# Performance work log

Measured on AMD Instinct MI355X. Metric: run time of the kernel, lower is better.

Reference implementation:

```python
import jax, jax.numpy as jnp
import numpy as np

B, T, C, H = 4, 2048, 1024, 16


def setup_inputs() -> dict:
    key = jax.random.key(0)
    k0, k1, k2 = jax.random.split(key, 3)
    s = C ** -0.5
    return {
        "x": jax.random.normal(k0, (B, T, C), jnp.float32),
        "Wqkv": jax.random.normal(k1, (C, 3 * C), jnp.float32) * s,
        "bqkv": jnp.zeros((3 * C,), jnp.float32),
        "Wo": jax.random.normal(k2, (C, C), jnp.float32) * s,
        "bo": jnp.zeros((C,), jnp.float32),
        "decoder": 1,
    }


def reference(x, Wqkv, bqkv, Wo, bo, decoder):
    Bx, Tx, Cx = x.shape
    d = Cx // H  # head dim
    qkv = x @ Wqkv + bqkv  # [B,T,3C]
    q, k, v = jnp.split(qkv, 3, axis=-1)
    q = q.reshape(Bx, Tx, H, d).transpose(0, 2, 1, 3)  # [B,H,T,d]
    k = k.reshape(Bx, Tx, H, d).transpose(0, 2, 1, 3)
    v = v.reshape(Bx, Tx, H, d).transpose(0, 2, 1, 3)
    # Source: qk / embd_dim**(-0.5)  ==  qk * sqrt(embd_dim)  (faithful quirk)
    scale = jnp.asarray(Cx ** 0.5, x.dtype)
    qk = jnp.einsum("bhqd,bhkd->bhqk", q, k) * scale  # [B,H,T,T]
    if decoder:  # decoder is a Python int constant
        tril = jnp.tril(jnp.ones((Tx, Tx), bool))
        qk = jnp.where(tril, qk, -jnp.inf)
    attn = jax.nn.softmax(qk, axis=-1)
    out = jnp.einsum("bhqk,bhkd->bhqd", attn, v)  # [B,H,T,d]
    out = out.transpose(0, 2, 1, 3).reshape(Bx, Tx, Cx)
    return out @ Wo + bo
```

## Files before the change

### kernel.cpp

```cpp
#include <hip/hip_runtime.h>
#include <cstdint>
#include <cstddef>

#define T_SEQ 2048
#define CEMB  1024
#define NHEAD 16
#define DHEAD 64

typedef __attribute__((ext_vector_type(8))) short bf16x8;
typedef __attribute__((ext_vector_type(4))) float f32x4;

static __device__ __forceinline__ unsigned short f2bf(float x) {
    unsigned u = __builtin_bit_cast(unsigned, x);
    unsigned r = (u + 0x7FFFu + ((u >> 16) & 1u)) >> 16;
    return (unsigned short)r;
}
static __device__ __forceinline__ float bf2f(unsigned short b) {
    unsigned u = ((unsigned)b) << 16;
    return __builtin_bit_cast(float, u);
}

static __device__ __forceinline__ void gload16(const short* gsrc, short* ldsbase) {
    __builtin_amdgcn_global_load_lds(
        (const __attribute__((address_space(1))) void*)gsrc,
        (__attribute__((address_space(3))) void*)ldsbase, 16, 0, 0);
}

template<int SPLIT, bool A_F32, bool OUT_BF16>
__global__ __launch_bounds__(256) void gemm_mfma_kernel(
    const float* __restrict__ Af,
    const short* __restrict__ Ah,
    const short* __restrict__ Bh,
    const short* __restrict__ Bl,
    const float* __restrict__ bias,
    void* __restrict__ Cout, int K, int ldc)
{
    __shared__ __align__(16) short smem[(SPLIT == 3) ? 16384 : 8192];

    const int tid = threadIdx.x;
    const int w = tid >> 6, l = tid & 63;
    const int lr = l & 15, lg = l >> 4;
    const int wr = w >> 1, wc = w & 1;
    const int row0 = blockIdx.y * 128;
    const int col0 = blockIdx.x * 128;

    f32x4 acc[4][4];
    #pragma unroll
    for (int mt = 0; mt < 4; ++mt)
        #pragma unroll
        for (int nt = 0; nt < 4; ++nt)
            acc[mt][nt] = (f32x4){0.f, 0.f, 0.f, 0.f};

    const int sB0 = w * 128 + l, sB1 = sB0 + 64;
    const short* gB0 = Bh + (size_t)(col0 + (sB0 & 127)) * K + (sB0 >> 7) * 8;
    const short* gB1 = Bh + (size_t)(col0 + (sB1 & 127)) * K + (sB1 >> 7) * 8;
    short* dB0 = &smem[4096 + (w * 128) * 8];
    short* dB1 = &smem[4096 + (w * 128 + 64) * 8];
    const short* gBl0 = nullptr; const short* gBl1 = nullptr;
    if constexpr (SPLIT == 3) {
        gBl0 = Bl + (size_t)(col0 + (sB0 & 127)) * K + (sB0 >> 7) * 8;
        gBl1 = Bl + (size_t)(col0 + (sB1 & 127)) * K + (sB1 >> 7) * 8;
    }

    const short* gA0 = nullptr; const short* gA1 = nullptr;
    if constexpr (!A_F32) {
        gA0 = Ah + (size_t)(row0 + (sB0 & 127)) * K + (sB0 >> 7) * 8;
        gA1 = Ah + (size_t)(row0 + (sB1 & 127)) * K + (sB1 >> 7) * 8;
    }
    short* dA0 = &smem[(w * 128) * 8];
    short* dA1 = &smem[(w * 128 + 64) * 8];

    const int arow = tid >> 1, ahalf = tid & 1;
    const float* gAf = A_F32 ? (Af + (size_t)(row0 + arow) * K + ahalf * 16) : nullptr;

    for (int kt = 0; kt < K; kt += 32) {
        __syncthreads();
        if constexpr (!A_F32) {
            gload16(gA0 + kt, dA0);
            gload16(gA1 + kt, dA1);
        }
        gload16(gB0 + kt, dB0);
        gload16(gB1 + kt, dB1);
        if constexpr (SPLIT == 3) {
            gload16(gBl0 + kt, &smem[12288 + (w * 128) * 8]);
            gload16(gBl1 + kt, &smem[12288 + (w * 128 + 64) * 8]);
        }
        if constexpr (A_F32) {
            const float* src = gAf + kt;
            float4 f0 = *(const float4*)(src);
            float4 f1 = *(const float4*)(src + 4);
            float4 f2 = *(const float4*)(src + 8);
            float4 f3 = *(const float4*)(src + 12);
            float xs[16] = {f0.x, f0.y, f0.z, f0.w, f1.x, f1.y, f1.z, f1.w,
                            f2.x, f2.y, f2.z, f2.w, f3.x, f3.y, f3.z, f3.w};
            #pragma unroll
            for (int q = 0; q < 2; ++q) {
                bf16x8 h8, l8;
                #pragma unroll
                for (int e = 0; e < 8; ++e) {
                    float x = xs[q * 8 + e];
                    if constexpr (SPLIT == 3) {
                        unsigned u = __builtin_bit_cast(unsigned, x);
                        h8[e] = (short)(unsigned short)(u >> 16);
                        float hf = __builtin_bit_cast(float, u & 0xFFFF0000u);
                        l8[e] = (short)f2bf(x - hf);
                    } else {
                        h8[e] = (short)f2bf(x);
                    }
                }
                int slot = (ahalf * 2 + q) * 128 + arow;
                *(bf16x8*)&smem[slot * 8] = h8;
                if constexpr (SPLIT == 3) *(bf16x8*)&smem[8192 + slot * 8] = l8;
            }
        }
        __syncthreads();

        const int aoff = (lg * 128 + wr * 64 + lr) * 8;
        const int boff = 4096 + (lg * 128 + wc * 64 + lr) * 8;
        bf16x8 ahf[4], alf[4];
        #pragma unroll
        for (int mt = 0; mt < 4; ++mt) {
            ahf[mt] = *(const bf16x8*)&smem[aoff + mt * 128];
            if constexpr (SPLIT == 3)
                alf[mt] = *(const bf16x8*)&smem[8192 + aoff + mt * 128];
        }
        #pragma unroll
        for (int nt = 0; nt < 4; ++nt) {
            bf16x8 bhf = *(const bf16x8*)&smem[boff + nt * 128];
            if constexpr (SPLIT == 3) {
                bf16x8 blf = *(const bf16x8*)&smem[8192 + boff + nt * 128];
                #pragma unroll
                for (int mt = 0; mt < 4; ++mt) {
                    acc[mt][nt] = __builtin_amdgcn_mfma_f32_16x16x32_bf16(ahf[mt], bhf, acc[mt][nt], 0, 0, 0);
                    acc[mt][nt] = __builtin_amdgcn_mfma_f32_16x16x32_bf16(alf[mt], bhf, acc[mt][nt], 0, 0, 0);
                    acc[mt][nt] = __builtin_amdgcn_mfma_f32_16x16x32_bf16(ahf[mt], blf, acc[mt][nt], 0, 0, 0);
                }
            } else {
                #pragma unroll
                for (int mt = 0; mt < 4; ++mt)
                    acc[mt][nt] = __builtin_amdgcn_mfma_f32_16x16x32_bf16(ahf[mt], bhf, acc[mt][nt], 0, 0, 0);
            }
        }
    }

    #pragma unroll
    for (int mt = 0; mt < 4; ++mt) {
        #pragma unroll
        for (int r = 0; r < 4; ++r) {
            int m = row0 + wr * 64 + mt * 16 + lg * 4 + r;
            #pragma unroll
            for (int nt = 0; nt < 4; ++nt) {
                int n = col0 + wc * 64 + nt * 16 + lr;
                float v = acc[mt][nt][r] + bias[n];
                if constexpr (OUT_BF16)
                    ((short*)Cout)[(size_t)m * ldc + n] = (short)f2bf(v);
                else
                    ((float*)Cout)[(size_t)m * ldc + n] = v;
            }
        }
    }
}

__global__ __launch_bounds__(256) void transpose_split_kernel(
    const float* __restrict__ src, int nsrc,
    short* __restrict__ hi, short* __restrict__ lo)
{
    __shared__ float tile[64][68];
    const int tid = threadIdx.x;
    const int n0 = blockIdx.x * 64, k0 = blockIdx.y * 64;
    {
        int kr = tid >> 2, cg = tid & 3;
        const float* s = src + (size_t)(k0 + kr) * nsrc + n0 + cg * 16;
        #pragma unroll
        for (int q = 0; q < 4; ++q) {
            float4 f = *(const float4*)(s + q * 4);
            tile[kr][cg * 16 + q * 4 + 0] = f.x;
            tile[kr][cg * 16 + q * 4 + 1] = f.y;
            tile[kr][cg * 16 + q * 4 + 2] = f.z;
            tile[kr][cg * 16 + q * 4 + 3] = f.w;
        }
    }
    __syncthreads();
    {
        int nr = tid >> 2, kg = tid & 3;
        int n = n0 + nr;
        bf16x8 h0, h1, lo0, lo1;
        #pragma unroll
        for (int e = 0; e < 8; ++e) {
            float a = tile[kg * 16 + e][nr];
            float b = tile[kg * 16 + 8 + e][nr];
            unsigned short ha = f2bf(a), hb = f2bf(b);
            h0[e] = (short)ha; h1[e] = (short)hb;
            lo0[e] = (short)f2bf(a - bf2f(ha));
            lo1[e] = (short)f2bf(b - bf2f(hb));
        }
        short* dh = hi + (size_t)n * 1024 + k0 + kg * 16;
        *(bf16x8*)dh = h0;
        *(bf16x8*)(dh + 8) = h1;
        if (lo) {
            short* dl = lo + (size_t)n * 1024 + k0 + kg * 16;
            *(bf16x8*)dl = lo0;
            *(bf16x8*)(dl + 8) = lo1;
        }
    }
}

__global__ __launch_bounds__(256) void repack_vt_kernel(
    const short* __restrict__ v, short* __restrict__ vt)
{
    __shared__ short tile[64][80];
    const int tid = threadIdx.x;
    const int tt = blockIdx.x, h = blockIdx.y, b = blockIdx.z;
    const int t0 = tt * 64;
    {
        int tr = tid >> 2, cgrp = tid & 3;
        const short* src = v + (size_t)(b * T_SEQ + t0 + tr) * CEMB + h * DHEAD + cgrp * 16;
        *(bf16x8*)&tile[tr][cgrp * 16]     = *(const bf16x8*)src;
        *(bf16x8*)&tile[tr][cgrp * 16 + 8] = *(const bf16x8*)(src + 8);
    }
    __syncthreads();
    {
        int d = tid >> 2, tc = tid & 3;
        short s[16];
        #pragma unroll
        for (int e = 0; e < 16; ++e) s[e] = tile[tc * 16 + e][d];
        short* dst = vt + ((size_t)((b * NHEAD + h) * DHEAD + d)) * T_SEQ + t0 + tc * 16;
        bf16x8 v0, v1;
        #pragma unroll
        for (int e = 0; e < 8; ++e) { v0[e] = s[e]; v1[e] = s[8 + e]; }
        *(bf16x8*)dst       = v0;
        *(bf16x8*)(dst + 8) = v1;
    }
}

__global__ __launch_bounds__(256) void attn_mfma_kernel(
    const float* __restrict__ qk, const short* __restrict__ vt,
    short* __restrict__ ctxb)
{
    __shared__ __align__(16) short K_hi[64 * 64];
    __shared__ __align__(16) short K_lo[64 * 64];
    __shared__ __align__(16) short Vs[64 * 64];
    __shared__ __align__(16) short Ps[4 * 32 * 64];

    const int tid = threadIdx.x;
    const int w   = tid >> 6;
    const int l   = tid & 63;
    const int lr  = l & 15;
    const int lg  = l >> 4;

    const int bid = blockIdx.x;
    const int pr  = bid & 7;
    const int bh  = bid >> 3;
    const int h   = bh & 15;
    const int b   = bh >> 4;

    const float* kglob = qk + (size_t)(b * T_SEQ) * 2048 + CEMB + h * DHEAD;
    const short* vglob = vt + ((size_t)((b * NHEAD + h) * DHEAD)) * T_SEQ;

    for (int half = 0; half < 2; ++half) {
        const int xi = half ? (15 - pr) : pr;
        const int q0 = xi * 128;
        const int qw = q0 + w * 32;

        bf16x8 ahi[2][2], alo[2][2];
        #pragma unroll
        for (int rt = 0; rt < 2; ++rt) {
            #pragma unroll
            for (int kk = 0; kk < 2; ++kk) {
                int row = qw + rt * 16 + lr;
                const float* qsrc = qk + (size_t)(b * T_SEQ + row) * 2048
                                      + h * DHEAD + kk * 32 + lg * 8;
                float4 fa = *(const float4*)qsrc;
                float4 fb = *(const float4*)(qsrc + 4);
                float v[8] = {fa.x, fa.y, fa.z, fa.w, fb.x, fb.y, fb.z, fb.w};
                #pragma unroll
                for (int e = 0; e < 8; ++e) {
                    float x = v[e] * 32.0f;
                    unsigned short hb = f2bf(x);
                    float hf = bf2f(hb);
                    unsigned short lb = f2bf(x - hf);
                    ahi[rt][kk][e] = (short)hb;
                    alo[rt][kk][e] = (short)lb;
                }
            }
        }

        f32x4 O[2][4];
        #pragma unroll
        for (int rt = 0; rt < 2; ++rt)
            #pragma unroll
            for (int dt = 0; dt < 4; ++dt)
                O[rt][dt] = (f32x4){0.f, 0.f, 0.f, 0.f};
        float mrun[2][4], lrun[2][4];
        #pragma unroll
        for (int rt = 0; rt < 2; ++rt)
            #pragma unroll
            for (int r = 0; r < 4; ++r) { mrun[rt][r] = -3.0e38f; lrun[rt][r] = 0.f; }

        const int nsteps = 2 * xi + 2;
        for (int t = 0; t < nsteps; ++t) {
            const int j0 = t * 64;
            __syncthreads();

            {
                int jr = tid >> 2;
                int cp = tid & 3;
                const float* ks = kglob + (size_t)(j0 + jr) * 2048 + cp * 16;
                float kv[16];
                #pragma unroll
                for (int q = 0; q < 4; ++q) {
                    float4 f = *(const float4*)(ks + q * 4);
                    kv[q * 4 + 0] = f.x; kv[q * 4 + 1] = f.y;
                    kv[q * 4 + 2] = f.z; kv[q * 4 + 3] = f.w;
                }
                #pragma unroll
                for (int c2 = 0; c2 < 2; ++c2) {
                    int chunk = cp * 2 + c2;
                    bf16x8 hv, lv;
                    #pragma unroll
                    for (int e = 0; e < 8; ++e) {
                        float x = kv[c2 * 8 + e];
                        unsigned short hb = f2bf(x);
                        float hf = bf2f(hb);
                        hv[e] = (short)hb;
                        lv[e] = (short)f2bf(x - hf);
                    }
                    int idx = jr * 64 + ((chunk ^ (jr & 7)) << 3);
                    *(bf16x8*)&K_hi[idx] = hv;
                    *(bf16x8*)&K_lo[idx] = lv;
                }
            }
            {
                int dr = tid >> 2;
                int vc = tid & 3;
                const short* vsrc = vglob + (size_t)dr * T_SEQ + j0 + vc * 16;
                bf16x8 v0 = *(const bf16x8*)vsrc;
                bf16x8 v1 = *(const bf16x8*)(vsrc + 8);
                int i0 = dr * 64 + (((vc * 2) ^ (dr & 7)) << 3);
                int i1 = dr * 64 + (((vc * 2 + 1) ^ (dr & 7)) << 3);
                *(bf16x8*)&Vs[i0] = v0;
                *(bf16x8*)&Vs[i1] = v1;
            }
            __syncthreads();

            #pragma unroll
            for (int rt = 0; rt < 2; ++rt) {
                f32x4 S[4];
                #pragma unroll
                for (int ct = 0; ct < 4; ++ct) {
                    f32x4 s = (f32x4){0.f, 0.f, 0.f, 0.f};
                    #pragma unroll
                    for (int kk = 0; kk < 2; ++kk) {
                        int j  = ct * 16 + lr;
                        int ck = kk * 4 + lg;
                        int idx = j * 64 + ((ck ^ (j & 7)) << 3);
                        bf16x8 bh8 = *(bf16x8*)&K_hi[idx];
                        bf16x8 bl8 = *(bf16x8*)&K_lo[idx];
                        s = __builtin_amdgcn_mfma_f32_16x16x32_bf16(ahi[rt][kk], bh8, s, 0, 0, 0);
                        s = __builtin_amdgcn_mfma_f32_16x16x32_bf16(alo[rt][kk], bh8, s, 0, 0, 0);
                        s = __builtin_amdgcn_mfma_f32_16x16x32_bf16(ahi[rt][kk], bl8, s, 0, 0, 0);
                    }
                    if (j0 + ct * 16 + 15 > qw + rt * 16) {
                        int jabs = j0 + ct * 16 + lr;
                        #pragma unroll
                        for (int r = 0; r < 4; ++r) {
                            int qabs = qw + rt * 16 + lg * 4 + r;
                            s[r] = (jabs <= qabs) ? s[r] : -3.0e38f;
                        }
                    }
                    S[ct] = s;
                }

                float mnew[4], alpha[4], lsum[4];
                #pragma unroll
                for (int r = 0; r < 4; ++r) {
                    float v = fmaxf(fmaxf(S[0][r], S[1][r]), fmaxf(S[2][r], S[3][r]));
                    v = fmaxf(v, __shfl_xor(v, 1));
                    v = fmaxf(v, __shfl_xor(v, 2));
                    v = fmaxf(v, __shfl_xor(v, 4));
                    v = fmaxf(v, __shfl_xor(v, 8));
                    mnew[r]  = fmaxf(mrun[rt][r], v);
                    alpha[r] = __expf(mrun[rt][r] - mnew[r]);
                    mrun[rt][r] = mnew[r];
                    lsum[r] = 0.f;
                }
                #pragma unroll
                for (int ct = 0; ct < 4; ++ct) {
                    #pragma unroll
                    for (int r = 0; r < 4; ++r) {
                        float p = __expf(S[ct][r] - mnew[r]);
                        lsum[r] += p;
                        int row = rt * 16 + lg * 4 + r;
                        int col = ct * 16 + lr;
                        Ps[w * 2048 + row * 64 + (col ^ ((row & 7) << 3))] = (short)f2bf(p);
                    }
                }
                #pragma unroll
                for (int r = 0; r < 4; ++r) {
                    float s = lsum[r];
                    s += __shfl_xor(s, 1);
                    s += __shfl_xor(s, 2);
                    s += __shfl_xor(s, 4);
                    s += __shfl_xor(s, 8);
                    lrun[rt][r] = lrun[rt][r] * alpha[r] + s;
                }
                #pragma unroll
                for (int dt = 0; dt < 4; ++dt)
                    #pragma unroll
                    for (int r = 0; r < 4; ++r)
                        O[rt][dt][r] *= alpha[r];
            }

            __builtin_amdgcn_wave_barrier();

            #pragma unroll
            for (int rt = 0; rt < 2; ++rt) {
                bf16x8 pa[2];
                #pragma unroll
                for (int jk = 0; jk < 2; ++jk) {
                    int row = rt * 16 + lr;
                    int ck  = jk * 4 + lg;
                    int idx = w * 2048 + row * 64 + ((ck ^ (row & 7)) << 3);
                    pa[jk] = *(bf16x8*)&Ps[idx];
                }
                #pragma unroll
                for (int dt = 0; dt < 4; ++dt) {
                    #pragma unroll
                    for (int jk = 0; jk < 2; ++jk) {
                        int d   = dt * 16 + lr;
                        int ck  = jk * 4 + lg;
                        int idx = d * 64 + ((ck ^ (d & 7)) << 3);
                        bf16x8 vb = *(bf16x8*)&Vs[idx];
                        O[rt][dt] = __builtin_amdgcn_mfma_f32_16x16x32_bf16(pa[jk], vb, O[rt][dt], 0, 0, 0);
                    }
                }
            }
        }

        #pragma unroll
        for (int rt = 0; rt < 2; ++rt) {
            #pragma unroll
            for (int r = 0; r < 4; ++r) {
                float inv = 1.0f / lrun[rt][r];
                int row = qw + rt * 16 + lg * 4 + r;
                #pragma unroll
                for (int dt = 0; dt < 4; ++dt) {
                    int col = h * DHEAD + dt * 16 + lr;
                    ctxb[(size_t)(b * T_SEQ + row) * CEMB + col] = (short)f2bf(O[rt][dt][r] * inv);
                }
            }
        }
    }
}

extern "C" void kernel_launch(void* const* d_in, const int* in_sizes, int n_in,
                              void* d_out, int out_size, void* d_ws, size_t ws_size,
                              hipStream_t stream)
{
    const float* x    = (const float*)d_in[0];
    const float* Wqkv = (const float*)d_in[1];
    const float* bqkv = (const float*)d_in[2];
    const float* Wo   = (const float*)d_in[3];
    const float* bo   = (const float*)d_in[4];
    float* out = (float*)d_out;

    char* ws = (char*)d_ws;
    float* qk   = (float*)ws;
    short* vbuf = (short*)ws;
    short* Vt   = (short*)(ws + (size_t)(64u << 20));
    short* ctxb = (short*)(ws + (size_t)(80u << 20));
    short* WhiT = (short*)(ws + (size_t)(96u << 20));
    short* WloT = (short*)(ws + (size_t)(102u << 20));
    short* WoT  = (short*)(ws + (size_t)(108u << 20));

    transpose_split_kernel<<<dim3(48, 16), 256, 0, stream>>>(Wqkv, 3 * CEMB, WhiT, WloT);
    transpose_split_kernel<<<dim3(16, 16), 256, 0, stream>>>(Wo, CEMB, WoT, nullptr);

    gemm_mfma_kernel<1, true, true><<<dim3(8, 64), 256, 0, stream>>>(
        x, nullptr, WhiT + (size_t)2048 * 1024, nullptr, bqkv + 2048, vbuf, CEMB, CEMB);

    repack_vt_kernel<<<dim3(32, 16, 4), 256, 0, stream>>>(vbuf, Vt);

    gemm_mfma_kernel<3, true, false><<<dim3(16, 64), 256, 0, stream>>>(
        x, nullptr, WhiT, WloT, bqkv, qk, CEMB, 2048);

    attn_mfma_kernel<<<dim3(512), 256, 0, stream>>>(qk, Vt, ctxb);

    gemm_mfma_kernel<1, false, false><<<dim3(8, 64), 256, 0, stream>>>(
        nullptr, ctxb, WoT, nullptr, bo, out, CEMB, CEMB);
}
```

Baseline: 391.4 us.

## Pre-split Q/K into bf16 hi/lo in GEMM epilogue and double-buffer attention loads

The QK projection GEMM now writes bf16 hi/lo halves directly, with the softmax scale times log2(e) folded into Q, instead of fp32 output. The attention kernel no longer converts fp32 to bf16 per tile. K and V tiles are streamed into double-buffered LDS with async global_load_lds, overlapping each load with compute on the previous tile. Masked row tiles are skipped, softmax uses exp2, and O and l are rescaled only when some row max increases. This cuts fp32 traffic and per-tile ALU conversion work, at the cost of more LDS and a truncation-based hi split.

```diff
diff --git a/kernel.cpp b/kernel.cpp
--- a/kernel.cpp
+++ b/kernel.cpp
@@ -7,6 +7,8 @@
 #define NHEAD 16
 #define DHEAD 64
 
+#define QSCALE 46.1662413084468f
+
 typedef __attribute__((ext_vector_type(8))) short bf16x8;
 typedef __attribute__((ext_vector_type(4))) float f32x4;
 
@@ -26,14 +28,12 @@
         (__attribute__((address_space(3))) void*)ldsbase, 16, 0, 0);
 }
 
-template<int SPLIT, bool A_F32, bool OUT_BF16>
+template<int SPLIT, bool A_F32, int OUT_MODE>
 __global__ __launch_bounds__(256) void gemm_mfma_kernel(
-    const float* __restrict__ Af,
-    const short* __restrict__ Ah,
-    const short* __restrict__ Bh,
-    const short* __restrict__ Bl,
+    const float* __restrict__ Af, const short* __restrict__ Ah,
+    const short* __restrict__ Bh, const short* __restrict__ Bl,
     const float* __restrict__ bias,
-    void* __restrict__ Cout, int K, int ldc)
+    void* __restrict__ Cout, void* __restrict__ Cout2, int K, int ldc)
 {
     __shared__ __align__(16) short smem[(SPLIT == 3) ? 16384 : 8192];
 
@@ -61,7 +61,6 @@
         gBl0 = Bl + (size_t)(col0 + (sB0 & 127)) * K + (sB0 >> 7) * 8;
         gBl1 = Bl + (size_t)(col0 + (sB1 & 127)) * K + (sB1 >> 7) * 8;
     }
-
     const short* gA0 = nullptr; const short* gA1 = nullptr;
     if constexpr (!A_F32) {
         gA0 = Ah + (size_t)(row0 + (sB0 & 127)) * K + (sB0 >> 7) * 8;
@@ -152,10 +151,17 @@
             for (int nt = 0; nt < 4; ++nt) {
                 int n = col0 + wc * 64 + nt * 16 + lr;
                 float v = acc[mt][nt][r] + bias[n];
-                if constexpr (OUT_BF16)
+                if constexpr (OUT_MODE == 0) {
+                    ((float*)Cout)[(size_t)m * ldc + n] = v;
+                } else if constexpr (OUT_MODE == 1) {
                     ((short*)Cout)[(size_t)m * ldc + n] = (short)f2bf(v);
-                else
-                    ((float*)Cout)[(size_t)m * ldc + n] = v;
+                } else {
+                    if (n < 1024) v *= QSCALE;
+                    unsigned u = __builtin_bit_cast(unsigned, v);
+                    ((short*)Cout)[(size_t)m * ldc + n] = (short)(unsigned short)(u >> 16);
+                    float hf = __builtin_bit_cast(float, u & 0xFFFF0000u);
+                    ((short*)Cout2)[(size_t)m * ldc + n] = (short)f2bf(v - hf);
+                }
             }
         }
     }
@@ -234,28 +240,25 @@
 }
 
 __global__ __launch_bounds__(256) void attn_mfma_kernel(
-    const float* __restrict__ qk, const short* __restrict__ vt,
-    short* __restrict__ ctxb)
+    const short* __restrict__ qkhi, const short* __restrict__ qklo,
+    const short* __restrict__ vt, short* __restrict__ ctxb)
 {
-    __shared__ __align__(16) short K_hi[64 * 64];
-    __shared__ __align__(16) short K_lo[64 * 64];
-    __shared__ __align__(16) short Vs[64 * 64];
-    __shared__ __align__(16) short Ps[4 * 32 * 64];
+    __shared__ __align__(16) short smem[32768];
 
     const int tid = threadIdx.x;
-    const int w   = tid >> 6;
-    const int l   = tid & 63;
-    const int lr  = l & 15;
-    const int lg  = l >> 4;
+    const int w = tid >> 6, l = tid & 63;
+    const int lr = l & 15, lg = l >> 4;
 
     const int bid = blockIdx.x;
-    const int pr  = bid & 7;
-    const int bh  = bid >> 3;
-    const int h   = bh & 15;
-    const int b   = bh >> 4;
-
-    const float* kglob = qk + (size_t)(b * T_SEQ) * 2048 + CEMB + h * DHEAD;
-    const short* vglob = vt + ((size_t)((b * NHEAD + h) * DHEAD)) * T_SEQ;
+    const int pr = bid & 7, bh = bid >> 3;
+    const int h = bh & 15, b = bh >> 4;
+    const size_t bT = (size_t)b * T_SEQ;
+
+    const int g0 = w * 128 + l, g1 = g0 + 64;
+    const int rg[2] = {g0 >> 3, g1 >> 3};
+    const int sc[2] = {(g0 & 7) ^ (rg[0] & 7), (g1 & 7) ^ (rg[1] & 7)};
+    short* const dst0 = &smem[(w * 128) * 8];
+    short* const dst1 = &smem[(w * 128 + 64) * 8];
 
     for (int half = 0; half < 2; ++half) {
         const int xi = half ? (15 - pr) : pr;
@@ -267,21 +270,9 @@
         for (int rt = 0; rt < 2; ++rt) {
             #pragma unroll
             for (int kk = 0; kk < 2; ++kk) {
-                int row = qw + rt * 16 + lr;
-                const float* qsrc = qk + (size_t)(b * T_SEQ + row) * 2048
-                                      + h * DHEAD + kk * 32 + lg * 8;
-                float4 fa = *(const float4*)qsrc;
-                float4 fb = *(const float4*)(qsrc + 4);
-                float v[8] = {fa.x, fa.y, fa.z, fa.w, fb.x, fb.y, fb.z, fb.w};
-                #pragma unroll
-                for (int e = 0; e < 8; ++e) {
-                    float x = v[e] * 32.0f;
-                    unsigned short hb = f2bf(x);
-                    float hf = bf2f(hb);
-                    unsigned short lb = f2bf(x - hf);
-                    ahi[rt][kk][e] = (short)hb;
-                    alo[rt][kk][e] = (short)lb;
-                }
+                size_t off = (bT + qw + rt * 16 + lr) * 2048 + h * DHEAD + kk * 32 + lg * 8;
+                ahi[rt][kk] = *(const bf16x8*)(qkhi + off);
+                alo[rt][kk] = *(const bf16x8*)(qklo + off);
             }
         }
 
@@ -297,54 +288,39 @@
             #pragma unroll
             for (int r = 0; r < 4; ++r) { mrun[rt][r] = -3.0e38f; lrun[rt][r] = 0.f; }
 
+        const short* pKh[2]; const short* pKl[2]; const short* pV[2];
+        #pragma unroll
+        for (int i = 0; i < 2; ++i) {
+            size_t koff = (bT + rg[i]) * 2048 + 1024 + h * DHEAD + sc[i] * 8;
+            pKh[i] = qkhi + koff;
+            pKl[i] = qklo + koff;
+            pV[i]  = vt + ((size_t)((b * NHEAD + h) * DHEAD) + rg[i]) * T_SEQ + sc[i] * 8;
+        }
+
+        #define STAGE(buf)  do {                                                  \
+            gload16(pKh[0], dst0 + (buf) * 4096);                                 \
+            gload16(pKh[1], dst1 + (buf) * 4096);                                 \
+            gload16(pKl[0], dst0 + 8192 + (buf) * 4096);                          \
+            gload16(pKl[1], dst1 + 8192 + (buf) * 4096);                          \
+            gload16(pV[0],  dst0 + 16384 + (buf) * 4096);                         \
+            gload16(pV[1],  dst1 + 16384 + (buf) * 4096);                         \
+            pKh[0] += 64 * 2048; pKh[1] += 64 * 2048;                             \
+            pKl[0] += 64 * 2048; pKl[1] += 64 * 2048;                             \
+            pV[0]  += 64;        pV[1]  += 64;                                    \
+        } while (0)
+
         const int nsteps = 2 * xi + 2;
+        STAGE(0);
         for (int t = 0; t < nsteps; ++t) {
             const int j0 = t * 64;
             __syncthreads();
-
-            {
-                int jr = tid >> 2;
-                int cp = tid & 3;
-                const float* ks = kglob + (size_t)(j0 + jr) * 2048 + cp * 16;
-                float kv[16];
-                #pragma unroll
-                for (int q = 0; q < 4; ++q) {
-                    float4 f = *(const float4*)(ks + q * 4);
-                    kv[q * 4 + 0] = f.x; kv[q * 4 + 1] = f.y;
-                    kv[q * 4 + 2] = f.z; kv[q * 4 + 3] = f.w;
-                }
-                #pragma unroll
-                for (int c2 = 0; c2 < 2; ++c2) {
-                    int chunk = cp * 2 + c2;
-                    bf16x8 hv, lv;
-                    #pragma unroll
-                    for (int e = 0; e < 8; ++e) {
-                        float x = kv[c2 * 8 + e];
-                        unsigned short hb = f2bf(x);
-                        float hf = bf2f(hb);
-                        hv[e] = (short)hb;
-                        lv[e] = (short)f2bf(x - hf);
-                    }
-                    int idx = jr * 64 + ((chunk ^ (jr & 7)) << 3);
-                    *(bf16x8*)&K_hi[idx] = hv;
-                    *(bf16x8*)&K_lo[idx] = lv;
-                }
-            }
-            {
-                int dr = tid >> 2;
-                int vc = tid & 3;
-                const short* vsrc = vglob + (size_t)dr * T_SEQ + j0 + vc * 16;
-                bf16x8 v0 = *(const bf16x8*)vsrc;
-                bf16x8 v1 = *(const bf16x8*)(vsrc + 8);
-                int i0 = dr * 64 + (((vc * 2) ^ (dr & 7)) << 3);
-                int i1 = dr * 64 + (((vc * 2 + 1) ^ (dr & 7)) << 3);
-                *(bf16x8*)&Vs[i0] = v0;
-                *(bf16x8*)&Vs[i1] = v1;
-            }
-            __syncthreads();
+            if (t + 1 < nsteps) STAGE((t + 1) & 1);
+            const int kb = (t & 1) * 4096;
 
             #pragma unroll
             for (int rt = 0; rt < 2; ++rt) {
+                if (j0 > qw + rt * 16 + 15) continue;
+
                 f32x4 S[4];
                 #pragma unroll
                 for (int ct = 0; ct < 4; ++ct) {
@@ -353,9 +329,9 @@
                     for (int kk = 0; kk < 2; ++kk) {
                         int j  = ct * 16 + lr;
                         int ck = kk * 4 + lg;
-                        int idx = j * 64 + ((ck ^ (j & 7)) << 3);
-                        bf16x8 bh8 = *(bf16x8*)&K_hi[idx];
-                        bf16x8 bl8 = *(bf16x8*)&K_lo[idx];
+                        int idx = kb + j * 64 + ((ck ^ (j & 7)) << 3);
+                        bf16x8 bh8 = *(bf16x8*)&smem[idx];
+                        bf16x8 bl8 = *(bf16x8*)&smem[8192 + idx];
                         s = __builtin_amdgcn_mfma_f32_16x16x32_bf16(ahi[rt][kk], bh8, s, 0, 0, 0);
                         s = __builtin_amdgcn_mfma_f32_16x16x32_bf16(alo[rt][kk], bh8, s, 0, 0, 0);
                         s = __builtin_amdgcn_mfma_f32_16x16x32_bf16(ahi[rt][kk], bl8, s, 0, 0, 0);
@@ -371,7 +347,7 @@
                     S[ct] = s;
                 }
 
-                float mnew[4], alpha[4], lsum[4];
+                float tm[4];
                 #pragma unroll
                 for (int r = 0; r < 4; ++r) {
                     float v = fmaxf(fmaxf(S[0][r], S[1][r]), fmaxf(S[2][r], S[3][r]));
@@ -379,20 +355,33 @@
                     v = fmaxf(v, __shfl_xor(v, 2));
                     v = fmaxf(v, __shfl_xor(v, 4));
                     v = fmaxf(v, __shfl_xor(v, 8));
-                    mnew[r]  = fmaxf(mrun[rt][r], v);
-                    alpha[r] = __expf(mrun[rt][r] - mnew[r]);
-                    mrun[rt][r] = mnew[r];
-                    lsum[r] = 0.f;
-                }
+                    tm[r] = v;
+                }
+                bool exceed = (tm[0] > mrun[rt][0]) | (tm[1] > mrun[rt][1]) |
+                              (tm[2] > mrun[rt][2]) | (tm[3] > mrun[rt][3]);
+                if (__any(exceed)) {
+                    #pragma unroll
+                    for (int r = 0; r < 4; ++r) {
+                        float mnew  = fmaxf(mrun[rt][r], tm[r]);
+                        float alpha = __builtin_amdgcn_exp2f(mrun[rt][r] - mnew);
+                        mrun[rt][r] = mnew;
+                        lrun[rt][r] *= alpha;
+                        #pragma unroll
+                        for (int dt = 0; dt < 4; ++dt)
+                            O[rt][dt][r] *= alpha;
+                    }
+                }
+
+                float lsum[4] = {0.f, 0.f, 0.f, 0.f};
                 #pragma unroll
                 for (int ct = 0; ct < 4; ++ct) {
                     #pragma unroll
                     for (int r = 0; r < 4; ++r) {
-                        float p = __expf(S[ct][r] - mnew[r]);
+                        float p = __builtin_amdgcn_exp2f(S[ct][r] - mrun[rt][r]);
                         lsum[r] += p;
                         int row = rt * 16 + lg * 4 + r;
                         int col = ct * 16 + lr;
-                        Ps[w * 2048 + row * 64 + (col ^ ((row & 7) << 3))] = (short)f2bf(p);
+                        smem[24576 + w * 2048 + row * 64 + (col ^ ((row & 7) << 3))] = (short)f2bf(p);
                     }
                 }
                 #pragma unroll
@@ -402,26 +391,21 @@
                     s += __shfl_xor(s, 2);
                     s += __shfl_xor(s, 4);
                     s += __shfl_xor(s, 8);
-                    lrun[rt][r] = lrun[rt][r] * alpha[r] + s;
-                }
-                #pragma unroll
-                for (int dt = 0; dt < 4; ++dt)
-                    #pragma unroll
-                    for (int r = 0; r < 4; ++r)
-                        O[rt][dt][r] *= alpha[r];
+                    lrun[rt][r] += s;
+                }
             }
 
             __builtin_amdgcn_wave_barrier();
 
             #pragma unroll
             for (int rt = 0; rt < 2; ++rt) {
+                if (j0 > qw + rt * 16 + 15) continue;
                 bf16x8 pa[2];
                 #pragma unroll
                 for (int jk = 0; jk < 2; ++jk) {
                     int row = rt * 16 + lr;
                     int ck  = jk * 4 + lg;
-                    int idx = w * 2048 + row * 64 + ((ck ^ (row & 7)) << 3);
-                    pa[jk] = *(bf16x8*)&Ps[idx];
+                    pa[jk] = *(bf16x8*)&smem[24576 + w * 2048 + row * 64 + ((ck ^ (row & 7)) << 3)];
                 }
                 #pragma unroll
                 for (int dt = 0; dt < 4; ++dt) {
@@ -429,13 +413,13 @@
                     for (int jk = 0; jk < 2; ++jk) {
                         int d   = dt * 16 + lr;
                         int ck  = jk * 4 + lg;
-                        int idx = d * 64 + ((ck ^ (d & 7)) << 3);
-                        bf16x8 vb = *(bf16x8*)&Vs[idx];
+                        bf16x8 vb = *(bf16x8*)&smem[16384 + kb + d * 64 + ((ck ^ (d & 7)) << 3)];
                         O[rt][dt] = __builtin_amdgcn_mfma_f32_16x16x32_bf16(pa[jk], vb, O[rt][dt], 0, 0, 0);
                     }
                 }
             }
         }
+        #undef STAGE
 
         #pragma unroll
         for (int rt = 0; rt < 2; ++rt) {
@@ -465,27 +449,30 @@
     float* out = (float*)d_out;
 
     char* ws = (char*)d_ws;
-    float* qk   = (float*)ws;
+    short* qkhi = (short*)ws;
     short* vbuf = (short*)ws;
+    short* qklo = (short*)(ws + (size_t)(32u << 20));
     short* Vt   = (short*)(ws + (size_t)(64u << 20));
     short* ctxb = (short*)(ws + (size_t)(80u << 20));
     short* WhiT = (short*)(ws + (size_t)(96u << 20));
     short* WloT = (short*)(ws + (size_t)(102u << 20));
     short* WoT  = (short*)(ws + (size_t)(108u << 20));
 
+    const int M = 4 * T_SEQ;
+
     transpose_split_kernel<<<dim3(48, 16), 256, 0, stream>>>(Wqkv, 3 * CEMB, WhiT, WloT);
     transpose_split_kernel<<<dim3(16, 16), 256, 0, stream>>>(Wo, CEMB, WoT, nullptr);
 
-    gemm_mfma_kernel<1, true, true><<<dim3(8, 64), 256, 0, stream>>>(
-        x, nullptr, WhiT + (size_t)2048 * 1024, nullptr, bqkv + 2048, vbuf, CEMB, CEMB);
+    gemm_mfma_kernel<1, true, 1><<<dim3(8, 64), 256, 0, stream>>>(
+        x, nullptr, WhiT + (size_t)2048 * 1024, nullptr, bqkv + 2048, vbuf, nullptr, CEMB, CEMB);
 
     repack_vt_kernel<<<dim3(32, 16, 4), 256, 0, stream>>>(vbuf, Vt);
 
-    gemm_mfma_kernel<3, true, false><<<dim3(16, 64), 256, 0, stream>>>(
-        x, nullptr, WhiT, WloT, bqkv, qk, CEMB, 2048);
-
-    attn_mfma_kernel<<<dim3(512), 256, 0, stream>>>(qk, Vt, ctxb);
-
-    gemm_mfma_kernel<1, false, false><<<dim3(8, 64), 256, 0, stream>>>(
-        nullptr, ctxb, WoT, nullptr, bo, out, CEMB, CEMB);
-}
+    gemm_mfma_kernel<3, true, 2><<<dim3(16, 64), 256, 0, stream>>>(
+        x, nullptr, WhiT, WloT, bqkv, qkhi, qklo, CEMB, 2048);
+
+    attn_mfma_kernel<<<dim3(512), 256, 0, stream>>>(qkhi, qklo, Vt, ctxb);
+
+    gemm_mfma_kernel<1, false, 0><<<dim3(8, 64), 256, 0, stream>>>(
+        nullptr, ctxb, WoT, nullptr, bo, out, nullptr, CEMB, CEMB);
+}
```

Measured after the change: 478.5 us. 22.3% more time.
